# Optimization experiments

Hardware: AMD Instinct MI355X
Metric: run time of the kernel (lower is better)

The kernel has to match this reference:

```python
import jax, jax.numpy as jnp
import numpy as np

EPS = 1e-6

def l2norm(x):
    # kernel.normalize: L2-normalize along the last (head_dim) axis
    return x * jax.lax.rsqrt(jnp.sum(x * x, axis=-1, keepdims=True) + EPS)

def setup_inputs() -> dict:
    key = jax.random.key(0)
    kq, kk, kv = jax.random.split(key, 3)
    B, H, S, D = 2, 12, 2048, 64
    Q = jax.random.normal(kq, (B, H, S, D), dtype=jnp.float32)
    K = jax.random.normal(kk, (B, H, S, D), dtype=jnp.float32)
    V = jax.random.normal(kv, (B, H, S, D), dtype=jnp.float32)
    mask = jnp.ones((B, S), dtype=jnp.int32)
    return {"Q": Q, "K": K, "V": V, "mask": mask, "hashcode_len": 9}

def reference(Q, K, V, mask, hashcode_len):
    # YOSO expectation kernel (num_hash_f < 0 path):
    #   Qn, Kn = L2-normalize(Q), L2-normalize(K)
    #   W[i,j] = (1 - arccos(<q_i, k_j>)/pi) ** hashcode_len   (collision prob of LSH)
    #   X = W @ V with key/query masking, then L2-normalize X.
    Qn = l2norm(Q)                                 # [B,H,S,D]
    Kn = l2norm(K)
    m = mask.astype(Q.dtype)                       # [B,S]
    sim = jnp.einsum('bhsd,bhtd->bhst', Qn, Kn)    # cosine similarities in [-1,1]
    sim = jnp.clip(sim, -1.0 + EPS, 1.0 - EPS)
    w = (1.0 - jnp.arccos(sim) / jnp.pi) ** hashcode_len   # [B,H,S,S]
    w = w * m[:, None, None, :]                    # mask keys
    X = jnp.einsum('bhst,bhtd->bhsd', w, V)        # [B,H,S,D]
    X = X * m[:, None, :, None]                    # mask queries
    X = l2norm(X)                                  # kernel.normalize(X)
    return X
```

## Files before the change

kernel.cpp:

```cpp
#include <hip/hip_runtime.h>
#include <hip/hip_bf16.h>
#include <hip/hip_fp16.h>

typedef short bf16x8 __attribute__((ext_vector_type(8)));
typedef _Float16 h8 __attribute__((ext_vector_type(8)));
typedef _Float16 h2v __attribute__((ext_vector_type(2)));
typedef __fp16 fp16x2 __attribute__((ext_vector_type(2)));
typedef float f32x16 __attribute__((ext_vector_type(16)));
typedef unsigned int uint32;

#define S 2048
#define D 64
#define NBH 24

#define GLOAD16(g, l) __builtin_amdgcn_global_load_lds(                      \
    (const __attribute__((address_space(1))) unsigned int*)(g),              \
    (__attribute__((address_space(3))) unsigned int*)(l), 16, 0, 0)

__device__ __forceinline__ int cvtpk_bf16(float lo, float hi) {
    int r;
    asm("v_cvt_pk_bf16_f32 %0, %1, %2" : "=v"(r) : "v"(lo), "v"(hi));
    return r;
}

__global__ __launch_bounds__(256) void prep(const float* __restrict__ Q,
                                            const float* __restrict__ K,
                                            const float* __restrict__ V,
                                            const int* __restrict__ mask,
                                            __hip_bfloat16* __restrict__ Qn,
                                            __hip_bfloat16* __restrict__ Kn,
                                            __half* __restrict__ Vt) {
    __shared__ float tile[64][65];
    const int NBQK = 2 * NBH * S / 16;
    int blk = blockIdx.x;
    int t = threadIdx.x;
    if (blk < NBQK) {
        int l16 = t & 15;
        int row = blk * 16 + (t >> 4);
        int half = row >= NBH * S;
        const float* in = half ? K : Q;
        __hip_bfloat16* out = half ? Kn : Qn;
        row -= half * NBH * S;
        float4 x = *(const float4*)(in + (size_t)row * 64 + l16 * 4);
        float ss = x.x * x.x + x.y * x.y + x.z * x.z + x.w * x.w;
        #pragma unroll
        for (int m = 1; m <= 8; m <<= 1) ss += __shfl_xor(ss, m, 64);
        float sc = rsqrtf(ss + 1e-6f);
        int2 pk = { cvtpk_bf16(x.x * sc, x.y * sc), cvtpk_bf16(x.z * sc, x.w * sc) };
        *(int2*)(out + (size_t)row * 64 + l16 * 4) = pk;
        return;
    }
    blk -= NBQK;
    int bh = blk >> 5;
    int b  = bh / 12;
    int s0 = (blk & 31) << 6;
    #pragma unroll
    for (int i = 0; i < 16; ++i) {
        int idx = i * 256 + t;
        int sl = idx >> 6, d = idx & 63;
        float mv = (float)mask[b * S + s0 + sl];
        tile[sl][d] = V[(size_t)bh * S * D + (size_t)(s0 + sl) * D + d] * mv;
    }
    __syncthreads();
    #pragma unroll
    for (int i = 0; i < 16; ++i) {
        int idx = i * 256 + t;
        int d = idx >> 6, sl = idx & 63;
        Vt[(size_t)bh * S * D + (size_t)d * S + s0 + sl] = __float2half(tile[sl][d]);
    }
}

template<int SPLITS>
__global__ __launch_bounds__(512) void yoso_main(const __hip_bfloat16* __restrict__ Qn,
                                                 const __hip_bfloat16* __restrict__ Kn,
                                                 const __half* __restrict__ Vt,
                                                 const int* __restrict__ mask,
                                                 const int* __restrict__ hlen_ptr,
                                                 void* __restrict__ outp) {
    __shared__ char lds[2][16384];

    const int QT = 8;
    const int blk = blockIdx.x;
    const int bh  = blk / (QT * SPLITS);
    const int rr  = blk % (QT * SPLITS);
    const int q0  = (rr / SPLITS) << 8;
    const int kq  = rr % SPLITS;
    const int kbase = kq * (S / SPLITS);
    const int NTt   = S / SPLITS / 64;

    const int b    = bh / 12;
    const int t    = threadIdx.x;
    const int w    = t >> 6;
    const int lane = t & 63;
    const int h    = lane >> 5;
    const int c31  = lane & 31;
    const int hcode = hlen_ptr[0];
    const size_t head = (size_t)bh * S * D;

    const int s_  = lane & 7;
    const int r3l = lane >> 3;
    const int e1  = s_ ^ r3l ^ (w & 7);
    const int u1  = e1 ^ ((e1 & 1) << 2);
    const int kgo1 = (8 * w + r3l) * 128 + u1 * 16;
    const int vgo1 = (8 * w + r3l) * 4096 + u1 * 16;
    const char* Kg = (const char*)(Kn + head);
    const char* Vg = (const char*)(Vt + head);

    char* ldsc = &lds[0][0];
    int koffs[2][4], voffs[2][2][2];
    #pragma unroll
    for (int kh2 = 0; kh2 < 2; ++kh2) {
        int krow = kh2 * 32 + c31;
        int kb3  = (krow & 7) ^ (krow >> 3) ^ (h << 2) ^ h;
        #pragma unroll
        for (int kd = 0; kd < 4; ++kd)
            koffs[kh2][kd] = krow * 128 + (((2 * kd) ^ kb3)) * 16;
        int vb3 = (c31 & 7) ^ (c31 >> 3) ^ (h << 2) ^ h ^ (kh2 << 2);
        #pragma unroll
        for (int kb2 = 0; kb2 < 2; ++kb2) {
            voffs[kh2][kb2][0] = c31 * 128        + (((kb2 << 1) ^ vb3)) * 16     + 8192;
            voffs[kh2][kb2][1] = (32 + c31) * 128 + (((kb2 << 1) ^ vb3 ^ 4)) * 16 + 8192;
        }
    }

    bf16x8 qf[4];
    {
        const __hip_bfloat16* qp = Qn + head + (size_t)(q0 + w * 32 + c31) * D + h * 8;
        qf[0] = *(const bf16x8*)(qp);
        qf[1] = *(const bf16x8*)(qp + 16);
        qf[2] = *(const bf16x8*)(qp + 32);
        qf[3] = *(const bf16x8*)(qp + 48);
    }
    asm volatile("" :: "v"(qf[0]), "v"(qf[1]), "v"(qf[2]), "v"(qf[3]));

    const f32x16 z16 = {0,0,0,0,0,0,0,0,0,0,0,0,0,0,0,0};
    f32x16 xacc0 = z16, xacc1 = z16;

    const bool  p9 = (hcode == 9);
    const float hf = (float)hcode;

    const h2v one2  = {(_Float16)1.0f,  (_Float16)1.0f};
    const h2v half2 = {(_Float16)0.5f,  (_Float16)0.5f};
    const h2v zero2 = {(_Float16)0.0f,  (_Float16)0.0f};
    const h2v q3c = {(_Float16)-0.00596128f, (_Float16)-0.00596128f};
    const h2v q2c = {(_Float16)-0.00575336f, (_Float16)-0.00575336f};
    const h2v q1c = {(_Float16)-0.03812704f, (_Float16)-0.03812704f};
    const h2v q0c = {(_Float16)-0.4501324f,  (_Float16)-0.4501324f};

    auto STAGE = [&](int base, int k0) {
        const char* kb = Kg + (size_t)k0 * 128;
        const char* vb = Vg + (size_t)k0 * 2;
        char* Kl = ldsc + base;
        char* Vl = Kl + 8192;
        GLOAD16(kb + kgo1, Kl + w * 1024);
        GLOAD16(vb + vgo1, Vl + w * 1024);
    };

    auto XFgen = [&](float s) -> float {
        float z  = fmaxf(1.0f - fabsf(s), 0.0f);
        float qp = ((0.00596128f * z + 0.00575336f) * z + 0.03812704f) * z + 0.4501324f;
        float tp = 0.5f - __builtin_amdgcn_sqrtf(z) * qp;
        float x  = 0.5f + __builtin_copysignf(tp, s);
        return __builtin_amdgcn_exp2f(hf * __builtin_amdgcn_logf(x));
    };

    auto COMPUTE = [&](int bufbase) {
        const char* base = ldsc + bufbase;
        #pragma unroll
        for (int kh2 = 0; kh2 < 2; ++kh2) {
            __builtin_amdgcn_s_setprio(1);
            f32x16 sacc = __builtin_amdgcn_mfma_f32_32x32x16_bf16(
                *(const bf16x8*)(base + koffs[kh2][0]), qf[0], z16, 0, 0, 0);
            #pragma unroll
            for (int kd = 1; kd < 4; ++kd)
                sacc = __builtin_amdgcn_mfma_f32_32x32x16_bf16(
                    *(const bf16x8*)(base + koffs[kh2][kd]), qf[kd], sacc, 0, 0, 0);
            __builtin_amdgcn_s_setprio(0);

            int u_[8];
            union HU { h2v v; fp16x2 p; uint32 u; };
            if (p9) {
                #pragma unroll
                for (int i = 0; i < 8; ++i) {
                    HU cv; cv.p = __builtin_amdgcn_cvt_pkrtz(sacc[2 * i], sacc[2 * i + 1]);
                    uint32 spb = cv.u;
                    HU za; za.u = spb & 0x7FFF7FFFu;
                    h2v z = one2 - za.v;
                    z = __builtin_elementwise_max(z, zero2);
                    h2v rt = __builtin_elementwise_sqrt(z);
                    h2v q = q3c * z + q2c;
                    q = q * z + q1c;
                    q = q * z + q0c;
                    HU tb; tb.v = q * rt + half2;
                    HU xb; xb.u = (tb.u & 0x7FFF7FFFu) | (spb & 0x80008000u);
                    h2v x = xb.v + half2;
                    h2v x2 = x * x;
                    h2v x4 = x2 * x2;
                    h2v x8 = x4 * x4;
                    HU wr; wr.v = x8 * x;
                    u_[i] = (int)wr.u;
                }
            } else {
                #pragma unroll
                for (int i = 0; i < 8; ++i) {
                    HU cv;
                    cv.p = __builtin_amdgcn_cvt_pkrtz(XFgen(sacc[2 * i]),
                                                      XFgen(sacc[2 * i + 1]));
                    u_[i] = (int)cv.u;
                }
            }
            asm("v_permlane32_swap_b32 %0, %1" : "+v"(u_[0]), "+v"(u_[2]));
            asm("v_permlane32_swap_b32 %0, %1" : "+v"(u_[1]), "+v"(u_[3]));
            asm("v_permlane32_swap_b32 %0, %1" : "+v"(u_[4]), "+v"(u_[6]));
            asm("v_permlane32_swap_b32 %0, %1" : "+v"(u_[5]), "+v"(u_[7]));
            union { int i[4]; h8 v; } f0, f1;
            f0.i[0] = u_[0]; f0.i[1] = u_[1]; f0.i[2] = u_[2]; f0.i[3] = u_[3];
            f1.i[0] = u_[4]; f1.i[1] = u_[5]; f1.i[2] = u_[6]; f1.i[3] = u_[7];

            h8 vf00 = *(const h8*)(base + voffs[kh2][0][0]);
            h8 vf01 = *(const h8*)(base + voffs[kh2][0][1]);
            h8 vf10 = *(const h8*)(base + voffs[kh2][1][0]);
            h8 vf11 = *(const h8*)(base + voffs[kh2][1][1]);
            __builtin_amdgcn_s_setprio(1);
            xacc0 = __builtin_amdgcn_mfma_f32_32x32x16_f16(f0.v, vf00, xacc0, 0, 0, 0);
            xacc1 = __builtin_amdgcn_mfma_f32_32x32x16_f16(f0.v, vf01, xacc1, 0, 0, 0);
            xacc0 = __builtin_amdgcn_mfma_f32_32x32x16_f16(f1.v, vf10, xacc0, 0, 0, 0);
            xacc1 = __builtin_amdgcn_mfma_f32_32x32x16_f16(f1.v, vf11, xacc1, 0, 0, 0);
            __builtin_amdgcn_s_setprio(0);
        }
    };

    STAGE(0, kbase);
    for (int t2 = 0; t2 < NTt; ++t2) {
        asm volatile("s_waitcnt vmcnt(0)" ::: "memory");
        __builtin_amdgcn_s_barrier();
        if (t2 + 1 < NTt) STAGE(((t2 + 1) & 1) * 16384, kbase + (t2 + 1) * 64);
        COMPUTE((t2 & 1) * 16384);
    }

    #pragma unroll
    for (int r = 0; r < 16; ++r) {
        int q  = (r & 3) + 8 * (r >> 2) + 4 * h;
        int qg = q0 + w * 32 + q;
        if (SPLITS > 1) {
            __half* pp = (__half*)outp + ((size_t)(kq * NBH + bh) * S + qg) * D;
            pp[c31]      = __float2half(xacc0[r]);
            pp[32 + c31] = __float2half(xacc1[r]);
        } else {
            float mq = (float)mask[b * S + qg];
            float x0 = xacc0[r] * mq, x1 = xacc1[r] * mq;
            float ss = x0 * x0 + x1 * x1;
            #pragma unroll
            for (int m = 1; m <= 16; m <<= 1) ss += __shfl_xor(ss, m, 64);
            float sc = rsqrtf(ss + 1e-6f);
            float* op = (float*)outp + ((size_t)bh * S + qg) * D;
            op[c31]      = x0 * sc;
            op[32 + c31] = x1 * sc;
        }
    }
}

template<int SPLITS>
__global__ __launch_bounds__(256) void combine_norm(const __half* __restrict__ P,
                                                    const int* __restrict__ mask,
                                                    float* __restrict__ out) {
    int t = threadIdx.x;
    int l16 = t & 15;
    size_t row = (size_t)blockIdx.x * 16 + (t >> 4);
    size_t i = row * 64 + l16 * 4;
    float x0 = 0.f, x1 = 0.f, x2 = 0.f, x3 = 0.f;
    #pragma unroll
    for (int k = 0; k < SPLITS; ++k) {
        const __half2* p2 = (const __half2*)(P + (size_t)k * NBH * S * D + i);
        __half2 ab = p2[0], cd = p2[1];
        x0 += __low2float(ab); x1 += __high2float(ab);
        x2 += __low2float(cd); x3 += __high2float(cd);
    }
    int bh = (int)(row >> 11);
    int sidx = (int)(row & 2047);
    int b = bh / 12;
    float mq = (float)mask[b * S + sidx];
    x0 *= mq; x1 *= mq; x2 *= mq; x3 *= mq;
    float ss = x0 * x0 + x1 * x1 + x2 * x2 + x3 * x3;
    #pragma unroll
    for (int m = 1; m <= 8; m <<= 1) ss += __shfl_xor(ss, m, 64);
    float sc = rsqrtf(ss + 1e-6f);
    float4 o = { x0 * sc, x1 * sc, x2 * sc, x3 * sc };
    *(float4*)(out + i) = o;
}

extern "C" void kernel_launch(void* const* d_in, const int* in_sizes, int n_in,
                              void* d_out, int out_size, void* d_ws, size_t ws_size,
                              hipStream_t stream) {
    const float* Q    = (const float*)d_in[0];
    const float* K    = (const float*)d_in[1];
    const float* V    = (const float*)d_in[2];
    const int*   mask = (const int*)d_in[3];
    const int*   hlen = (const int*)d_in[4];
    float*       out  = (float*)d_out;

    __hip_bfloat16* Qn = (__hip_bfloat16*)d_ws;
    __hip_bfloat16* Kn = Qn + (size_t)NBH * S * D;
    __half*         Vt = (__half*)(Kn + (size_t)NBH * S * D);
    __half* Pbuf = (__half*)((char*)d_ws + 3ull * NBH * S * D * 2);

    const size_t base_b = 3ull * NBH * S * D * 2;
    const size_t part_h = (size_t)NBH * S * D * 2;

    prep<<<2 * NBH * S / 16 + NBH * 32, 256, 0, stream>>>(Q, K, V, mask, Qn, Kn, Vt);
    if (ws_size >= base_b + 4 * part_h) {
        yoso_main<4><<<NBH * 8 * 4, 512, 0, stream>>>(Qn, Kn, Vt, mask, hlen, Pbuf);
        combine_norm<4><<<NBH * S / 16, 256, 0, stream>>>(Pbuf, mask, out);
    } else if (ws_size >= base_b + 2 * part_h) {
        yoso_main<2><<<NBH * 8 * 2, 512, 0, stream>>>(Qn, Kn, Vt, mask, hlen, Pbuf);
        combine_norm<2><<<NBH * S / 16, 256, 0, stream>>>(Pbuf, mask, out);
    } else {
        yoso_main<1><<<NBH * 8, 512, 0, stream>>>(Qn, Kn, Vt, mask, hlen, out);
    }
}
```

Before: 67.93 us.

## Split key tile across wave pairs with LDS reduction, halving query tile per block

Each block now covers 128 queries instead of 256. Waves are paired: the two waves in a pair share the same 32 query rows and each processes one half of every 64-key tile, so the unrolled two-pass loop inside COMPUTE goes away. At the end, the partial X accumulators of the paired waves are summed through LDS before being written out, and the grid doubles. The aim is more blocks and less serial work per wave, improving occupancy and latency hiding, at the cost of twice the K/V tile loading per query and an extra LDS reduction with two barriers.

```diff
diff --git a/kernel.cpp b/kernel.cpp
--- a/kernel.cpp
+++ b/kernel.cpp
@@ -79,11 +79,11 @@
                                                  void* __restrict__ outp) {
     __shared__ char lds[2][16384];
 
-    const int QT = 8;
+    const int QT = 16;
     const int blk = blockIdx.x;
     const int bh  = blk / (QT * SPLITS);
     const int rr  = blk % (QT * SPLITS);
-    const int q0  = (rr / SPLITS) << 8;
+    const int q0  = (rr / SPLITS) << 7;
     const int kq  = rr % SPLITS;
     const int kbase = kq * (S / SPLITS);
     const int NTt   = S / SPLITS / 64;
@@ -94,6 +94,8 @@
     const int lane = t & 63;
     const int h    = lane >> 5;
     const int c31  = lane & 31;
+    const int qh   = w >> 1;
+    const int kh   = w & 1;
     const int hcode = hlen_ptr[0];
     const size_t head = (size_t)bh * S * D;
 
@@ -107,25 +109,24 @@
     const char* Vg = (const char*)(Vt + head);
 
     char* ldsc = &lds[0][0];
-    int koffs[2][4], voffs[2][2][2];
-    #pragma unroll
-    for (int kh2 = 0; kh2 < 2; ++kh2) {
-        int krow = kh2 * 32 + c31;
+    int koffs[4], voffs[2][2];
+    {
+        int krow = kh * 32 + c31;
         int kb3  = (krow & 7) ^ (krow >> 3) ^ (h << 2) ^ h;
         #pragma unroll
         for (int kd = 0; kd < 4; ++kd)
-            koffs[kh2][kd] = krow * 128 + (((2 * kd) ^ kb3)) * 16;
-        int vb3 = (c31 & 7) ^ (c31 >> 3) ^ (h << 2) ^ h ^ (kh2 << 2);
+            koffs[kd] = krow * 128 + (((2 * kd) ^ kb3)) * 16;
+        int vb3 = (c31 & 7) ^ (c31 >> 3) ^ (h << 2) ^ h ^ (kh << 2);
         #pragma unroll
         for (int kb2 = 0; kb2 < 2; ++kb2) {
-            voffs[kh2][kb2][0] = c31 * 128        + (((kb2 << 1) ^ vb3)) * 16     + 8192;
-            voffs[kh2][kb2][1] = (32 + c31) * 128 + (((kb2 << 1) ^ vb3 ^ 4)) * 16 + 8192;
+            voffs[kb2][0] = c31 * 128        + (((kb2 << 1) ^ vb3)) * 16     + 8192;
+            voffs[kb2][1] = (32 + c31) * 128 + (((kb2 << 1) ^ vb3 ^ 4)) * 16 + 8192;
         }
     }
 
     bf16x8 qf[4];
     {
-        const __hip_bfloat16* qp = Qn + head + (size_t)(q0 + w * 32 + c31) * D + h * 8;
+        const __hip_bfloat16* qp = Qn + head + (size_t)(q0 + qh * 32 + c31) * D + h * 8;
         qf[0] = *(const bf16x8*)(qp);
         qf[1] = *(const bf16x8*)(qp + 16);
         qf[2] = *(const bf16x8*)(qp + 32);
@@ -166,68 +167,65 @@
 
     auto COMPUTE = [&](int bufbase) {
         const char* base = ldsc + bufbase;
-        #pragma unroll
-        for (int kh2 = 0; kh2 < 2; ++kh2) {
-            __builtin_amdgcn_s_setprio(1);
-            f32x16 sacc = __builtin_amdgcn_mfma_f32_32x32x16_bf16(
-                *(const bf16x8*)(base + koffs[kh2][0]), qf[0], z16, 0, 0, 0);
+        __builtin_amdgcn_s_setprio(1);
+        f32x16 sacc = __builtin_amdgcn_mfma_f32_32x32x16_bf16(
+            *(const bf16x8*)(base + koffs[0]), qf[0], z16, 0, 0, 0);
+        #pragma unroll
+        for (int kd = 1; kd < 4; ++kd)
+            sacc = __builtin_amdgcn_mfma_f32_32x32x16_bf16(
+                *(const bf16x8*)(base + koffs[kd]), qf[kd], sacc, 0, 0, 0);
+        __builtin_amdgcn_s_setprio(0);
+
+        int u_[8];
+        union HU { h2v v; fp16x2 p; uint32 u; };
+        if (p9) {
             #pragma unroll
-            for (int kd = 1; kd < 4; ++kd)
-                sacc = __builtin_amdgcn_mfma_f32_32x32x16_bf16(
-                    *(const bf16x8*)(base + koffs[kh2][kd]), qf[kd], sacc, 0, 0, 0);
-            __builtin_amdgcn_s_setprio(0);
-
-            int u_[8];
-            union HU { h2v v; fp16x2 p; uint32 u; };
-            if (p9) {
-                #pragma unroll
-                for (int i = 0; i < 8; ++i) {
-                    HU cv; cv.p = __builtin_amdgcn_cvt_pkrtz(sacc[2 * i], sacc[2 * i + 1]);
-                    uint32 spb = cv.u;
-                    HU za; za.u = spb & 0x7FFF7FFFu;
-                    h2v z = one2 - za.v;
-                    z = __builtin_elementwise_max(z, zero2);
-                    h2v rt = __builtin_elementwise_sqrt(z);
-                    h2v q = q3c * z + q2c;
-                    q = q * z + q1c;
-                    q = q * z + q0c;
-                    HU tb; tb.v = q * rt + half2;
-                    HU xb; xb.u = (tb.u & 0x7FFF7FFFu) | (spb & 0x80008000u);
-                    h2v x = xb.v + half2;
-                    h2v x2 = x * x;
-                    h2v x4 = x2 * x2;
-                    h2v x8 = x4 * x4;
-                    HU wr; wr.v = x8 * x;
-                    u_[i] = (int)wr.u;
-                }
-            } else {
-                #pragma unroll
-                for (int i = 0; i < 8; ++i) {
-                    HU cv;
-                    cv.p = __builtin_amdgcn_cvt_pkrtz(XFgen(sacc[2 * i]),
-                                                      XFgen(sacc[2 * i + 1]));
-                    u_[i] = (int)cv.u;
-                }
+            for (int i = 0; i < 8; ++i) {
+                HU cv; cv.p = __builtin_amdgcn_cvt_pkrtz(sacc[2 * i], sacc[2 * i + 1]);
+                uint32 spb = cv.u;
+                HU za; za.u = spb & 0x7FFF7FFFu;
+                h2v z = one2 - za.v;
+                z = __builtin_elementwise_max(z, zero2);
+                h2v rt = __builtin_elementwise_sqrt(z);
+                h2v q = q3c * z + q2c;
+                q = q * z + q1c;
+                q = q * z + q0c;
+                HU tb; tb.v = q * rt + half2;
+                HU xb; xb.u = (tb.u & 0x7FFF7FFFu) | (spb & 0x80008000u);
+                h2v x = xb.v + half2;
+                h2v x2 = x * x;
+                h2v x4 = x2 * x2;
+                h2v x8 = x4 * x4;
+                HU wr; wr.v = x8 * x;
+                u_[i] = (int)wr.u;
             }
-            asm("v_permlane32_swap_b32 %0, %1" : "+v"(u_[0]), "+v"(u_[2]));
-            asm("v_permlane32_swap_b32 %0, %1" : "+v"(u_[1]), "+v"(u_[3]));
-            asm("v_permlane32_swap_b32 %0, %1" : "+v"(u_[4]), "+v"(u_[6]));
-            asm("v_permlane32_swap_b32 %0, %1" : "+v"(u_[5]), "+v"(u_[7]));
-            union { int i[4]; h8 v; } f0, f1;
-            f0.i[0] = u_[0]; f0.i[1] = u_[1]; f0.i[2] = u_[2]; f0.i[3] = u_[3];
-            f1.i[0] = u_[4]; f1.i[1] = u_[5]; f1.i[2] = u_[6]; f1.i[3] = u_[7];
-
-            h8 vf00 = *(const h8*)(base + voffs[kh2][0][0]);
-            h8 vf01 = *(const h8*)(base + voffs[kh2][0][1]);
-            h8 vf10 = *(const h8*)(base + voffs[kh2][1][0]);
-            h8 vf11 = *(const h8*)(base + voffs[kh2][1][1]);
-            __builtin_amdgcn_s_setprio(1);
-            xacc0 = __builtin_amdgcn_mfma_f32_32x32x16_f16(f0.v, vf00, xacc0, 0, 0, 0);
-            xacc1 = __builtin_amdgcn_mfma_f32_32x32x16_f16(f0.v, vf01, xacc1, 0, 0, 0);
-            xacc0 = __builtin_amdgcn_mfma_f32_32x32x16_f16(f1.v, vf10, xacc0, 0, 0, 0);
-            xacc1 = __builtin_amdgcn_mfma_f32_32x32x16_f16(f1.v, vf11, xacc1, 0, 0, 0);
-            __builtin_amdgcn_s_setprio(0);
+        } else {
+            #pragma unroll
+            for (int i = 0; i < 8; ++i) {
+                HU cv;
+                cv.p = __builtin_amdgcn_cvt_pkrtz(XFgen(sacc[2 * i]),
+                                                  XFgen(sacc[2 * i + 1]));
+                u_[i] = (int)cv.u;
+            }
         }
+        asm("v_permlane32_swap_b32 %0, %1" : "+v"(u_[0]), "+v"(u_[2]));
+        asm("v_permlane32_swap_b32 %0, %1" : "+v"(u_[1]), "+v"(u_[3]));
+        asm("v_permlane32_swap_b32 %0, %1" : "+v"(u_[4]), "+v"(u_[6]));
+        asm("v_permlane32_swap_b32 %0, %1" : "+v"(u_[5]), "+v"(u_[7]));
+        union { int i[4]; h8 v; } f0, f1;
+        f0.i[0] = u_[0]; f0.i[1] = u_[1]; f0.i[2] = u_[2]; f0.i[3] = u_[3];
+        f1.i[0] = u_[4]; f1.i[1] = u_[5]; f1.i[2] = u_[6]; f1.i[3] = u_[7];
+
+        h8 vf00 = *(const h8*)(base + voffs[0][0]);
+        h8 vf01 = *(const h8*)(base + voffs[0][1]);
+        h8 vf10 = *(const h8*)(base + voffs[1][0]);
+        h8 vf11 = *(const h8*)(base + voffs[1][1]);
+        __builtin_amdgcn_s_setprio(1);
+        xacc0 = __builtin_amdgcn_mfma_f32_32x32x16_f16(f0.v, vf00, xacc0, 0, 0, 0);
+        xacc1 = __builtin_amdgcn_mfma_f32_32x32x16_f16(f0.v, vf01, xacc1, 0, 0, 0);
+        xacc0 = __builtin_amdgcn_mfma_f32_32x32x16_f16(f1.v, vf10, xacc0, 0, 0, 0);
+        xacc1 = __builtin_amdgcn_mfma_f32_32x32x16_f16(f1.v, vf11, xacc1, 0, 0, 0);
+        __builtin_amdgcn_s_setprio(0);
     };
 
     STAGE(0, kbase);
@@ -238,24 +236,39 @@
         COMPUTE((t2 & 1) * 16384);
     }
 
-    #pragma unroll
-    for (int r = 0; r < 16; ++r) {
-        int q  = (r & 3) + 8 * (r >> 2) + 4 * h;
-        int qg = q0 + w * 32 + q;
-        if (SPLITS > 1) {
-            __half* pp = (__half*)outp + ((size_t)(kq * NBH + bh) * S + qg) * D;
-            pp[c31]      = __float2half(xacc0[r]);
-            pp[32 + c31] = __float2half(xacc1[r]);
-        } else {
-            float mq = (float)mask[b * S + qg];
-            float x0 = xacc0[r] * mq, x1 = xacc1[r] * mq;
-            float ss = x0 * x0 + x1 * x1;
-            #pragma unroll
-            for (int m = 1; m <= 16; m <<= 1) ss += __shfl_xor(ss, m, 64);
-            float sc = rsqrtf(ss + 1e-6f);
-            float* op = (float*)outp + ((size_t)bh * S + qg) * D;
-            op[c31]      = x0 * sc;
-            op[32 + c31] = x1 * sc;
+    __syncthreads();
+    float* red = (float*)ldsc;
+    if (kh == 1) {
+        #pragma unroll
+        for (int r = 0; r < 16; ++r) {
+            int q = (r & 3) + 8 * (r >> 2) + 4 * h;
+            red[(qh * 32 + q) * 64 + c31]      = xacc0[r];
+            red[(qh * 32 + q) * 64 + 32 + c31] = xacc1[r];
+        }
+    }
+    __syncthreads();
+    if (kh == 0) {
+        #pragma unroll
+        for (int r = 0; r < 16; ++r) {
+            int q  = (r & 3) + 8 * (r >> 2) + 4 * h;
+            int qg = q0 + qh * 32 + q;
+            float x0 = xacc0[r] + red[(qh * 32 + q) * 64 + c31];
+            float x1 = xacc1[r] + red[(qh * 32 + q) * 64 + 32 + c31];
+            if (SPLITS > 1) {
+                __half* pp = (__half*)outp + ((size_t)(kq * NBH + bh) * S + qg) * D;
+                pp[c31]      = __float2half(x0);
+                pp[32 + c31] = __float2half(x1);
+            } else {
+                float mq = (float)mask[b * S + qg];
+                x0 *= mq; x1 *= mq;
+                float ss = x0 * x0 + x1 * x1;
+                #pragma unroll
+                for (int m = 1; m <= 16; m <<= 1) ss += __shfl_xor(ss, m, 64);
+                float sc = rsqrtf(ss + 1e-6f);
+                float* op = (float*)outp + ((size_t)bh * S + qg) * D;
+                op[c31]      = x0 * sc;
+                op[32 + c31] = x1 * sc;
+            }
         }
     }
 }
@@ -309,12 +322,12 @@
 
     prep<<<2 * NBH * S / 16 + NBH * 32, 256, 0, stream>>>(Q, K, V, mask, Qn, Kn, Vt);
     if (ws_size >= base_b + 4 * part_h) {
-        yoso_main<4><<<NBH * 8 * 4, 512, 0, stream>>>(Qn, Kn, Vt, mask, hlen, Pbuf);
+        yoso_main<4><<<NBH * 16 * 4, 512, 0, stream>>>(Qn, Kn, Vt, mask, hlen, Pbuf);
         combine_norm<4><<<NBH * S / 16, 256, 0, stream>>>(Pbuf, mask, out);
     } else if (ws_size >= base_b + 2 * part_h) {
-        yoso_main<2><<<NBH * 8 * 2, 512, 0, stream>>>(Qn, Kn, Vt, mask, hlen, Pbuf);
+        yoso_main<2><<<NBH * 16 * 2, 512, 0, stream>>>(Qn, Kn, Vt, mask, hlen, Pbuf);
         combine_norm<2><<<NBH * S / 16, 256, 0, stream>>>(Pbuf, mask, out);
     } else {
-        yoso_main<1><<<NBH * 8, 512, 0, stream>>>(Qn, Kn, Vt, mask, hlen, out);
-    }
-}
+        yoso_main<1><<<NBH * 16, 512, 0, stream>>>(Qn, Kn, Vt, mask, hlen, out);
+    }
+}
```

Result: slower. 71.23 us (+4.9%).
